# Optimization experiments

Hardware: AMD Instinct MI355X
Metric: run time of the kernel (lower is better)

## Reference

```python
import jax, jax.numpy as jnp
import numpy as np

NEG_BIG = -9e15  # matches torch's -9000000000000000.0 mask value


def _l2norm(x, eps=1e-12):
    # F.normalize(x, p=2, dim=1)
    n = jnp.sqrt(jnp.sum(x * x, axis=1, keepdims=True))
    return x / jnp.maximum(n, eps)


def _fusion_attribute(emb, att_emb, adj):
    # cosine similarity [N, M]
    sim = _l2norm(emb) @ _l2norm(att_emb).T
    sim = sim * adj
    # masked softmax over dim=1: zeros -> -9e15
    logits = jnp.where(sim != 0, sim, jnp.full_like(sim, NEG_BIG))
    attention = jax.nn.softmax(logits, axis=1)
    return attention @ att_emb


def setup_inputs() -> dict:
    key = jax.random.key(0)
    k1, k2, k3, k4 = jax.random.split(key, 4)
    U, I, D = 10000, 8000, 64
    users_emb = 0.1 * jax.random.normal(k1, (U, D), dtype=jnp.float32)  # init.normal_(std=0.1)
    items_emb = 0.1 * jax.random.normal(k2, (I, D), dtype=jnp.float32)
    Out_UserAttNets = (jax.random.uniform(k3, (U, I)) < 0.05).astype(jnp.float32)
    Out_ItemAttNets = (jax.random.uniform(k4, (I, U)) < 0.05).astype(jnp.float32)
    return {
        "num_users": U,
        "num_items": I,
        "users_emb": users_emb,
        "items_emb": items_emb,
        "Out_UserAttNets": Out_UserAttNets,
        "Out_ItemAttNets": Out_ItemAttNets,
    }


def reference(num_users, num_items, users_emb, items_emb, Out_UserAttNets, Out_ItemAttNets):
    out_useratt_emb = _fusion_attribute(users_emb, items_emb, Out_UserAttNets)
    out_itematt_emb = _fusion_attribute(items_emb, users_emb, Out_ItemAttNets)
    return (users_emb, items_emb, out_useratt_emb, out_itematt_emb)
```

## Files before the change

kernel.cpp:

```cpp
#include <hip/hip_runtime.h>
#include <math.h>

typedef float f32x4 __attribute__((ext_vector_type(4)));

#define SEGCAP 768

__global__ __launch_bounds__(256) void rinv_kernel(const float* __restrict__ users,
                                                   const float* __restrict__ items,
                                                   float* __restrict__ rinvU,
                                                   float* __restrict__ rinvI,
                                                   int U, int I) {
    int lane = threadIdx.x & 63;
    int row  = (blockIdx.x << 2) + (threadIdx.x >> 6);
    const float* src; float* dst;
    if (row < U) {
        src = users + (size_t)row * 64; dst = rinvU + row;
    } else {
        int r = row - U; if (r >= I) return;
        src = items + (size_t)r * 64; dst = rinvI + r;
    }
    float x = src[lane];
    float s = x * x;
#pragma unroll
    for (int off = 32; off; off >>= 1) s += __shfl_xor(s, off, 64);
    if (lane == 0) *dst = 1.0f / fmaxf(sqrtf(s), 1e-12f);
}

__global__ __launch_bounds__(256) void att_dir_kernel(
    const float* __restrict__ qemb, const float* __restrict__ kvemb,
    const float* __restrict__ adj,  const float* __restrict__ rq,
    const float* __restrict__ rk,   float* __restrict__ outp,
    int N, int M)
{
    __shared__ int cols_sh[4][SEGCAP];

    const int lane = threadIdx.x & 63;
    const int wid  = threadIdx.x >> 6;
    const int wave0   = (blockIdx.x << 2) + wid;
    const int nwaves  = gridDim.x << 2;

    const int sub = lane & 15;
    const int grp = lane >> 4;
    const unsigned long long lt = (1ULL << lane) - 1ULL;
    const int M4 = M >> 2;
    const int* cp = cols_sh[wid];

    for (int row = wave0; row < N; row += nwaves) {
        const float* adjrow = adj + (size_t)row * M;

        int wcount = 0;
        for (int i4 = lane; i4 < M4; i4 += 64) {
            f32x4 a = __builtin_nontemporal_load((const f32x4*)adjrow + i4);
#pragma unroll
            for (int j = 0; j < 4; ++j) {
                bool pred = (a[j] != 0.0f);
                unsigned long long mask = __ballot(pred);
                if (pred) {
                    int pos = wcount + __popcll(mask & lt);
                    if (pos < SEGCAP) cols_sh[wid][pos] = (i4 << 2) + j;
                }
                wcount += __popcll(mask);
            }
        }
        wcount = __shfl(wcount, 0, 64);
        if (M & 3) {
            int idx = (M4 << 2) + lane;
            bool pred = (idx < M) && (adjrow[idx] != 0.0f);
            unsigned long long mask = __ballot(pred);
            if (pred) {
                int pos = wcount + __popcll(mask & lt);
                if (pos < SEGCAP) cols_sh[wid][pos] = idx;
            }
            wcount += __popcll(mask);
        }
        int cnt = wcount > SEGCAP ? SEGCAP : wcount;

        const float rqv = rq[row];
        f32x4 q4 = ((const f32x4*)(qemb + (size_t)row * 64))[sub] * rqv;

        f32x4 acc = (f32x4){0.f, 0.f, 0.f, 0.f};
        float wsum = 0.f;

        int i = grp;
        for (; i + 12 < cnt; i += 16) {
            int c0 = cp[i], c1 = cp[i + 4], c2 = cp[i + 8], c3 = cp[i + 12];
            float k0 = rk[c0], k1 = rk[c1], k2 = rk[c2], k3 = rk[c3];
            f32x4 r0 = ((const f32x4*)(kvemb + (size_t)c0 * 64))[sub];
            f32x4 r1 = ((const f32x4*)(kvemb + (size_t)c1 * 64))[sub];
            f32x4 r2 = ((const f32x4*)(kvemb + (size_t)c2 * 64))[sub];
            f32x4 r3 = ((const f32x4*)(kvemb + (size_t)c3 * 64))[sub];
            float d0 = 0.f, d1 = 0.f, d2 = 0.f, d3 = 0.f;
#pragma unroll
            for (int c = 0; c < 4; ++c) {
                d0 = fmaf(q4[c], r0[c], d0);
                d1 = fmaf(q4[c], r1[c], d1);
                d2 = fmaf(q4[c], r2[c], d2);
                d3 = fmaf(q4[c], r3[c], d3);
            }
#pragma unroll
            for (int off = 1; off <= 8; off <<= 1) {
                d0 += __shfl_xor(d0, off, 64);
                d1 += __shfl_xor(d1, off, 64);
                d2 += __shfl_xor(d2, off, 64);
                d3 += __shfl_xor(d3, off, 64);
            }
            float s0 = d0 * k0, s1 = d1 * k1, s2 = d2 * k2, s3 = d3 * k3;
            float w0 = (s0 != 0.0f) ? __expf(s0 - 1.0f) : 0.0f;
            float w1 = (s1 != 0.0f) ? __expf(s1 - 1.0f) : 0.0f;
            float w2 = (s2 != 0.0f) ? __expf(s2 - 1.0f) : 0.0f;
            float w3 = (s3 != 0.0f) ? __expf(s3 - 1.0f) : 0.0f;
#pragma unroll
            for (int c = 0; c < 4; ++c)
                acc[c] = fmaf(w0, r0[c], fmaf(w1, r1[c],
                         fmaf(w2, r2[c], fmaf(w3, r3[c], acc[c]))));
            if (sub == 0) wsum += (w0 + w1) + (w2 + w3);
        }
        for (; i < cnt; i += 4) {
            int c0 = cp[i];
            float k0 = rk[c0];
            f32x4 r0 = ((const f32x4*)(kvemb + (size_t)c0 * 64))[sub];
            float d0 = 0.f;
#pragma unroll
            for (int c = 0; c < 4; ++c) d0 = fmaf(q4[c], r0[c], d0);
#pragma unroll
            for (int off = 1; off <= 8; off <<= 1) d0 += __shfl_xor(d0, off, 64);
            float s0 = d0 * k0;
            float w0 = (s0 != 0.0f) ? __expf(s0 - 1.0f) : 0.0f;
#pragma unroll
            for (int c = 0; c < 4; ++c) acc[c] = fmaf(w0, r0[c], acc[c]);
            if (sub == 0) wsum += w0;
        }

#pragma unroll
        for (int off = 16; off <= 32; off <<= 1) {
            wsum += __shfl_xor(wsum, off, 64);
#pragma unroll
            for (int c = 0; c < 4; ++c) acc[c] += __shfl_xor(acc[c], off, 64);
        }
        float den = __shfl(wsum, 0, 64);

        if (lane < 16) {
            float* orow = outp + (size_t)row * 64;
            if (den > 0.0f) {
                ((f32x4*)orow)[lane] = acc * (1.0f / den);
            } else {
                f32x4 m = (f32x4){0.f, 0.f, 0.f, 0.f};
                for (int r = 0; r < M; ++r)
                    m += ((const f32x4*)(kvemb + (size_t)r * 64))[lane];
                ((f32x4*)orow)[lane] = m * (1.0f / (float)M);
            }
        }
    }
}

extern "C" void kernel_launch(void* const* d_in, const int* in_sizes, int n_in,
                              void* d_out, int out_size, void* d_ws, size_t ws_size,
                              hipStream_t stream) {
    const float* users = (const float*)d_in[2];
    const float* items = (const float*)d_in[3];
    const float* adjU  = (const float*)d_in[4];
    const float* adjI  = (const float*)d_in[5];
    const int U = in_sizes[2] / 64;
    const int I = in_sizes[3] / 64;

    float* out   = (float*)d_out;
    float* rinvU = (float*)d_ws;
    float* rinvI = rinvU + U;

    hipMemcpyAsync(out, users, (size_t)U * 64 * sizeof(float),
                   hipMemcpyDeviceToDevice, stream);
    hipMemcpyAsync(out + (size_t)U * 64, items, (size_t)I * 64 * sizeof(float),
                   hipMemcpyDeviceToDevice, stream);

    rinv_kernel<<<(U + I + 3) / 4, 256, 0, stream>>>(users, items, rinvU, rinvI, U, I);

    float* outUatt = out + (size_t)(U + I) * 64;
    float* outIatt = outUatt + (size_t)U * 64;

    int gU = (U + 3) / 4; if (gU > 2048) gU = 2048;
    int gI = (I + 3) / 4; if (gI > 2048) gI = 2048;
    att_dir_kernel<<<gU, 256, 0, stream>>>(users, items, adjU, rinvU, rinvI,
                                           outUatt, U, I);
    att_dir_kernel<<<gI, 256, 0, stream>>>(items, users, adjI, rinvI, rinvU,
                                           outIatt, I, U);
}
```

Before: 261.4 us.

## Store normalized embeddings as bf16 and merge both attention directions into one launch

The prep kernel now writes L2-normalized embeddings in bf16 along with per-row norms. The attention kernel gathers these half-size rows, uses them directly for the cosine dot, and rebuilds the raw value as hat times norm. Both directions are fused into one launch with one wave per row instead of a persistent grid-stride loop. This halves gather bandwidth and removes a launch, at the cost of bf16 rounding in both the similarity and the value accumulation, which may hurt accuracy.

```diff
diff --git a/kernel.cpp b/kernel.cpp
--- a/kernel.cpp
+++ b/kernel.cpp
@@ -2,153 +2,176 @@
 #include <math.h>
 
 typedef float f32x4 __attribute__((ext_vector_type(4)));
+typedef unsigned int u32;
+typedef u32 u32x2 __attribute__((ext_vector_type(2)));
+typedef unsigned short u16;
 
 #define SEGCAP 768
 
-__global__ __launch_bounds__(256) void rinv_kernel(const float* __restrict__ users,
-                                                   const float* __restrict__ items,
-                                                   float* __restrict__ rinvU,
-                                                   float* __restrict__ rinvI,
-                                                   int U, int I) {
+__device__ __forceinline__ u16 f2b(float x) {
+    union { float f; u32 u; } v; v.f = x;
+    return (u16)((v.u + 0x7FFFu + ((v.u >> 16) & 1u)) >> 16);
+}
+__device__ __forceinline__ float b2f_lo(u32 u) { union { u32 u; float f; } v; v.u = u << 16;         return v.f; }
+__device__ __forceinline__ float b2f_hi(u32 u) { union { u32 u; float f; } v; v.u = u & 0xFFFF0000u; return v.f; }
+
+__global__ __launch_bounds__(256) void prep_kernel(
+    const float* __restrict__ users, const float* __restrict__ items,
+    u16* __restrict__ hU, u16* __restrict__ hI,
+    float* __restrict__ nU, float* __restrict__ nI, int U, int I)
+{
     int lane = threadIdx.x & 63;
     int row  = (blockIdx.x << 2) + (threadIdx.x >> 6);
-    const float* src; float* dst;
-    if (row < U) {
-        src = users + (size_t)row * 64; dst = rinvU + row;
-    } else {
-        int r = row - U; if (r >= I) return;
-        src = items + (size_t)r * 64; dst = rinvI + r;
-    }
-    float x = src[lane];
+    const float* src; u16* hat; float* nrm; int r;
+    if (row < U) { r = row; src = users; hat = hU; nrm = nU; }
+    else { r = row - U; if (r >= I) return; src = items; hat = hI; nrm = nI; }
+    float x = src[(size_t)r * 64 + lane];
     float s = x * x;
 #pragma unroll
     for (int off = 32; off; off >>= 1) s += __shfl_xor(s, off, 64);
-    if (lane == 0) *dst = 1.0f / fmaxf(sqrtf(s), 1e-12f);
-}
-
-__global__ __launch_bounds__(256) void att_dir_kernel(
-    const float* __restrict__ qemb, const float* __restrict__ kvemb,
-    const float* __restrict__ adj,  const float* __restrict__ rq,
-    const float* __restrict__ rk,   float* __restrict__ outp,
-    int N, int M)
+    float nv   = sqrtf(s);
+    float rinv = 1.0f / fmaxf(nv, 1e-12f);
+    hat[(size_t)r * 64 + lane] = f2b(x * rinv);
+    if (lane == 0) nrm[r] = nv;
+}
+
+__global__ __launch_bounds__(256) void att_row_kernel(
+    const float* __restrict__ users, const float* __restrict__ items,
+    const u16* __restrict__ hU, const u16* __restrict__ hI,
+    const float* __restrict__ nU, const float* __restrict__ nI,
+    const float* __restrict__ adjU, const float* __restrict__ adjI,
+    float* __restrict__ outU, float* __restrict__ outI, int U, int I)
 {
     __shared__ int cols_sh[4][SEGCAP];
 
     const int lane = threadIdx.x & 63;
     const int wid  = threadIdx.x >> 6;
-    const int wave0   = (blockIdx.x << 2) + wid;
-    const int nwaves  = gridDim.x << 2;
-
-    const int sub = lane & 15;
-    const int grp = lane >> 4;
+    const int grow = (blockIdx.x << 2) + wid;
+    if (grow >= U + I) return;
+
+    const u16* qhat; const u16* kvhat; const float* kvnrm;
+    const float* kvraw; const float* adj; float* outp;
+    int M, row;
+    if (grow < U) {
+        row = grow;     qhat = hU; kvhat = hI; kvnrm = nI;
+        kvraw = items;  adj = adjU; outp = outU; M = I;
+    } else {
+        row = grow - U; qhat = hI; kvhat = hU; kvnrm = nU;
+        kvraw = users;  adj = adjI; outp = outI; M = U;
+    }
+    const float* adjrow = adj + (size_t)row * M;
+
+    int wcount = 0;
+    const int M4 = M >> 2;
     const unsigned long long lt = (1ULL << lane) - 1ULL;
-    const int M4 = M >> 2;
-    const int* cp = cols_sh[wid];
-
-    for (int row = wave0; row < N; row += nwaves) {
-        const float* adjrow = adj + (size_t)row * M;
-
-        int wcount = 0;
-        for (int i4 = lane; i4 < M4; i4 += 64) {
-            f32x4 a = __builtin_nontemporal_load((const f32x4*)adjrow + i4);
-#pragma unroll
-            for (int j = 0; j < 4; ++j) {
-                bool pred = (a[j] != 0.0f);
-                unsigned long long mask = __ballot(pred);
-                if (pred) {
-                    int pos = wcount + __popcll(mask & lt);
-                    if (pos < SEGCAP) cols_sh[wid][pos] = (i4 << 2) + j;
-                }
-                wcount += __popcll(mask);
-            }
-        }
-        wcount = __shfl(wcount, 0, 64);
-        if (M & 3) {
-            int idx = (M4 << 2) + lane;
-            bool pred = (idx < M) && (adjrow[idx] != 0.0f);
+    for (int i4 = lane; i4 < M4; i4 += 64) {
+        f32x4 a = __builtin_nontemporal_load((const f32x4*)adjrow + i4);
+#pragma unroll
+        for (int j = 0; j < 4; ++j) {
+            bool pred = (a[j] != 0.0f);
             unsigned long long mask = __ballot(pred);
             if (pred) {
                 int pos = wcount + __popcll(mask & lt);
-                if (pos < SEGCAP) cols_sh[wid][pos] = idx;
+                if (pos < SEGCAP) cols_sh[wid][pos] = (i4 << 2) + j;
             }
             wcount += __popcll(mask);
         }
-        int cnt = wcount > SEGCAP ? SEGCAP : wcount;
-
-        const float rqv = rq[row];
-        f32x4 q4 = ((const f32x4*)(qemb + (size_t)row * 64))[sub] * rqv;
-
-        f32x4 acc = (f32x4){0.f, 0.f, 0.f, 0.f};
-        float wsum = 0.f;
-
-        int i = grp;
-        for (; i + 12 < cnt; i += 16) {
-            int c0 = cp[i], c1 = cp[i + 4], c2 = cp[i + 8], c3 = cp[i + 12];
-            float k0 = rk[c0], k1 = rk[c1], k2 = rk[c2], k3 = rk[c3];
-            f32x4 r0 = ((const f32x4*)(kvemb + (size_t)c0 * 64))[sub];
-            f32x4 r1 = ((const f32x4*)(kvemb + (size_t)c1 * 64))[sub];
-            f32x4 r2 = ((const f32x4*)(kvemb + (size_t)c2 * 64))[sub];
-            f32x4 r3 = ((const f32x4*)(kvemb + (size_t)c3 * 64))[sub];
-            float d0 = 0.f, d1 = 0.f, d2 = 0.f, d3 = 0.f;
-#pragma unroll
-            for (int c = 0; c < 4; ++c) {
-                d0 = fmaf(q4[c], r0[c], d0);
-                d1 = fmaf(q4[c], r1[c], d1);
-                d2 = fmaf(q4[c], r2[c], d2);
-                d3 = fmaf(q4[c], r3[c], d3);
-            }
-#pragma unroll
-            for (int off = 1; off <= 8; off <<= 1) {
-                d0 += __shfl_xor(d0, off, 64);
-                d1 += __shfl_xor(d1, off, 64);
-                d2 += __shfl_xor(d2, off, 64);
-                d3 += __shfl_xor(d3, off, 64);
-            }
-            float s0 = d0 * k0, s1 = d1 * k1, s2 = d2 * k2, s3 = d3 * k3;
-            float w0 = (s0 != 0.0f) ? __expf(s0 - 1.0f) : 0.0f;
-            float w1 = (s1 != 0.0f) ? __expf(s1 - 1.0f) : 0.0f;
-            float w2 = (s2 != 0.0f) ? __expf(s2 - 1.0f) : 0.0f;
-            float w3 = (s3 != 0.0f) ? __expf(s3 - 1.0f) : 0.0f;
-#pragma unroll
-            for (int c = 0; c < 4; ++c)
-                acc[c] = fmaf(w0, r0[c], fmaf(w1, r1[c],
-                         fmaf(w2, r2[c], fmaf(w3, r3[c], acc[c]))));
-            if (sub == 0) wsum += (w0 + w1) + (w2 + w3);
-        }
-        for (; i < cnt; i += 4) {
-            int c0 = cp[i];
-            float k0 = rk[c0];
-            f32x4 r0 = ((const f32x4*)(kvemb + (size_t)c0 * 64))[sub];
-            float d0 = 0.f;
-#pragma unroll
-            for (int c = 0; c < 4; ++c) d0 = fmaf(q4[c], r0[c], d0);
-#pragma unroll
-            for (int off = 1; off <= 8; off <<= 1) d0 += __shfl_xor(d0, off, 64);
-            float s0 = d0 * k0;
-            float w0 = (s0 != 0.0f) ? __expf(s0 - 1.0f) : 0.0f;
-#pragma unroll
-            for (int c = 0; c < 4; ++c) acc[c] = fmaf(w0, r0[c], acc[c]);
-            if (sub == 0) wsum += w0;
-        }
-
-#pragma unroll
-        for (int off = 16; off <= 32; off <<= 1) {
-            wsum += __shfl_xor(wsum, off, 64);
-#pragma unroll
-            for (int c = 0; c < 4; ++c) acc[c] += __shfl_xor(acc[c], off, 64);
-        }
-        float den = __shfl(wsum, 0, 64);
-
-        if (lane < 16) {
-            float* orow = outp + (size_t)row * 64;
-            if (den > 0.0f) {
-                ((f32x4*)orow)[lane] = acc * (1.0f / den);
-            } else {
-                f32x4 m = (f32x4){0.f, 0.f, 0.f, 0.f};
-                for (int r = 0; r < M; ++r)
-                    m += ((const f32x4*)(kvemb + (size_t)r * 64))[lane];
-                ((f32x4*)orow)[lane] = m * (1.0f / (float)M);
-            }
+    }
+    wcount = __shfl(wcount, 0, 64);
+    if (M & 3) {
+        int idx = (M4 << 2) + lane;
+        bool pred = (idx < M) && (adjrow[idx] != 0.0f);
+        unsigned long long mask = __ballot(pred);
+        if (pred) {
+            int pos = wcount + __popcll(mask & lt);
+            if (pos < SEGCAP) cols_sh[wid][pos] = idx;
+        }
+        wcount += __popcll(mask);
+    }
+    int cnt = wcount > SEGCAP ? SEGCAP : wcount;
+
+    const int sub = lane & 15;
+    const int grp = lane >> 4;
+
+    u32x2 qw = *(const u32x2*)(qhat + (size_t)row * 64 + sub * 4);
+    const float q0 = b2f_lo(qw[0]), q1 = b2f_hi(qw[0]);
+    const float q2 = b2f_lo(qw[1]), q3 = b2f_hi(qw[1]);
+
+    float a0 = 0.f, a1 = 0.f, a2 = 0.f, a3 = 0.f, wsum = 0.f;
+    const int* cp = cols_sh[wid];
+
+    int i = grp;
+    for (; i + 12 < cnt; i += 16) {
+        int c0 = cp[i], c1 = cp[i + 4], c2 = cp[i + 8], c3 = cp[i + 12];
+        u32x2 v0 = *(const u32x2*)(kvhat + (size_t)c0 * 64 + sub * 4);
+        u32x2 v1 = *(const u32x2*)(kvhat + (size_t)c1 * 64 + sub * 4);
+        u32x2 v2 = *(const u32x2*)(kvhat + (size_t)c2 * 64 + sub * 4);
+        u32x2 v3 = *(const u32x2*)(kvhat + (size_t)c3 * 64 + sub * 4);
+        float n0 = kvnrm[c0], n1 = kvnrm[c1], n2 = kvnrm[c2], n3 = kvnrm[c3];
+        float r00 = b2f_lo(v0[0]), r01 = b2f_hi(v0[0]), r02 = b2f_lo(v0[1]), r03 = b2f_hi(v0[1]);
+        float r10 = b2f_lo(v1[0]), r11 = b2f_hi(v1[0]), r12 = b2f_lo(v1[1]), r13 = b2f_hi(v1[1]);
+        float r20 = b2f_lo(v2[0]), r21 = b2f_hi(v2[0]), r22 = b2f_lo(v2[1]), r23 = b2f_hi(v2[1]);
+        float r30 = b2f_lo(v3[0]), r31 = b2f_hi(v3[0]), r32 = b2f_lo(v3[1]), r33 = b2f_hi(v3[1]);
+        float d0 = fmaf(q0, r00, fmaf(q1, r01, fmaf(q2, r02, q3 * r03)));
+        float d1 = fmaf(q0, r10, fmaf(q1, r11, fmaf(q2, r12, q3 * r13)));
+        float d2 = fmaf(q0, r20, fmaf(q1, r21, fmaf(q2, r22, q3 * r23)));
+        float d3 = fmaf(q0, r30, fmaf(q1, r31, fmaf(q2, r32, q3 * r33)));
+#pragma unroll
+        for (int off = 1; off <= 8; off <<= 1) {
+            d0 += __shfl_xor(d0, off, 64);
+            d1 += __shfl_xor(d1, off, 64);
+            d2 += __shfl_xor(d2, off, 64);
+            d3 += __shfl_xor(d3, off, 64);
+        }
+        float w0 = (d0 != 0.0f) ? __expf(d0 - 1.0f) : 0.0f;
+        float w1 = (d1 != 0.0f) ? __expf(d1 - 1.0f) : 0.0f;
+        float w2 = (d2 != 0.0f) ? __expf(d2 - 1.0f) : 0.0f;
+        float w3 = (d3 != 0.0f) ? __expf(d3 - 1.0f) : 0.0f;
+        float x0 = w0 * n0, x1 = w1 * n1, x2 = w2 * n2, x3 = w3 * n3;
+        a0 = fmaf(x0, r00, fmaf(x1, r10, fmaf(x2, r20, fmaf(x3, r30, a0))));
+        a1 = fmaf(x0, r01, fmaf(x1, r11, fmaf(x2, r21, fmaf(x3, r31, a1))));
+        a2 = fmaf(x0, r02, fmaf(x1, r12, fmaf(x2, r22, fmaf(x3, r32, a2))));
+        a3 = fmaf(x0, r03, fmaf(x1, r13, fmaf(x2, r23, fmaf(x3, r33, a3))));
+        if (sub == 0) wsum += (w0 + w1) + (w2 + w3);
+    }
+    for (; i < cnt; i += 4) {
+        int c0 = cp[i];
+        u32x2 v0 = *(const u32x2*)(kvhat + (size_t)c0 * 64 + sub * 4);
+        float n0 = kvnrm[c0];
+        float r00 = b2f_lo(v0[0]), r01 = b2f_hi(v0[0]), r02 = b2f_lo(v0[1]), r03 = b2f_hi(v0[1]);
+        float d0 = fmaf(q0, r00, fmaf(q1, r01, fmaf(q2, r02, q3 * r03)));
+#pragma unroll
+        for (int off = 1; off <= 8; off <<= 1) d0 += __shfl_xor(d0, off, 64);
+        float w0 = (d0 != 0.0f) ? __expf(d0 - 1.0f) : 0.0f;
+        float x0 = w0 * n0;
+        a0 = fmaf(x0, r00, a0);
+        a1 = fmaf(x0, r01, a1);
+        a2 = fmaf(x0, r02, a2);
+        a3 = fmaf(x0, r03, a3);
+        if (sub == 0) wsum += w0;
+    }
+
+#pragma unroll
+    for (int off = 16; off <= 32; off <<= 1) {
+        wsum += __shfl_xor(wsum, off, 64);
+        a0 += __shfl_xor(a0, off, 64);
+        a1 += __shfl_xor(a1, off, 64);
+        a2 += __shfl_xor(a2, off, 64);
+        a3 += __shfl_xor(a3, off, 64);
+    }
+    float den = __shfl(wsum, 0, 64);
+
+    if (lane < 16) {
+        float* orow = outp + (size_t)row * 64;
+        if (den > 0.0f) {
+            float inv = 1.0f / den;
+            f32x4 o = (f32x4){a0 * inv, a1 * inv, a2 * inv, a3 * inv};
+            ((f32x4*)orow)[lane] = o;
+        } else {
+            f32x4 m = (f32x4){0.f, 0.f, 0.f, 0.f};
+            for (int r = 0; r < M; ++r)
+                m += ((const f32x4*)(kvraw + (size_t)r * 64))[lane];
+            ((f32x4*)orow)[lane] = m * (1.0f / (float)M);
         }
     }
 }
@@ -163,24 +186,23 @@
     const int U = in_sizes[2] / 64;
     const int I = in_sizes[3] / 64;
 
-    float* out   = (float*)d_out;
-    float* rinvU = (float*)d_ws;
-    float* rinvI = rinvU + U;
+    char* w = (char*)d_ws;
+    u16* hU = (u16*)w;    w += (size_t)U * 64 * sizeof(u16);
+    u16* hI = (u16*)w;    w += (size_t)I * 64 * sizeof(u16);
+    float* nU = (float*)w; w += (size_t)U * sizeof(float);
+    float* nI = (float*)w;
+
+    float* out = (float*)d_out;
 
     hipMemcpyAsync(out, users, (size_t)U * 64 * sizeof(float),
                    hipMemcpyDeviceToDevice, stream);
     hipMemcpyAsync(out + (size_t)U * 64, items, (size_t)I * 64 * sizeof(float),
                    hipMemcpyDeviceToDevice, stream);
 
-    rinv_kernel<<<(U + I + 3) / 4, 256, 0, stream>>>(users, items, rinvU, rinvI, U, I);
+    prep_kernel<<<(U + I + 3) / 4, 256, 0, stream>>>(users, items, hU, hI, nU, nI, U, I);
 
     float* outUatt = out + (size_t)(U + I) * 64;
     float* outIatt = outUatt + (size_t)U * 64;
-
-    int gU = (U + 3) / 4; if (gU > 2048) gU = 2048;
-    int gI = (I + 3) / 4; if (gI > 2048) gI = 2048;
-    att_dir_kernel<<<gU, 256, 0, stream>>>(users, items, adjU, rinvU, rinvI,
-                                           outUatt, U, I);
-    att_dir_kernel<<<gI, 256, 0, stream>>>(items, users, adjI, rinvI, rinvU,
-                                           outIatt, I, U);
-}
+    att_row_kernel<<<(U + I + 3) / 4, 256, 0, stream>>>(
+        users, items, hU, hI, nU, nI, adjU, adjI, outUatt, outIatt, U, I);
+}
```

Result: faster. 220.5 us (median of 2 runs) (-15.7%).
